# Performance work log

Hardware: AMD Instinct MI355X
Metric: run time of the kernel (lower is better)

The kernel has to match this reference:

```python
import jax, jax.numpy as jnp
import numpy as np

N_NODES = 50000


def _gcn_layer(x, src, dst, W, b, n_nodes):
    # x: [N, Cin] -> linear -> [N, Cout]
    h = x @ W.T + b
    # degree over destination (col) index, including self loops
    deg = jax.ops.segment_sum(jnp.ones(src.shape[0], dtype=x.dtype), dst,
                              num_segments=n_nodes)
    dinv = jnp.where(deg > 0, deg ** -0.5, jnp.zeros((), x.dtype))
    norm = dinv[src] * dinv[dst]                      # [E]
    msg = h[src] * norm[:, None]                      # gather + scale
    return jax.ops.segment_sum(msg, dst, num_segments=n_nodes)  # scatter-add


def setup_inputs() -> dict:
    key = jax.random.key(0)
    k1, k2, k3, k4, k5, k6 = jax.random.split(key, 6)
    num_features = 128
    hidden_dim = 128
    n_edges = 1_600_000
    x = jax.random.normal(k1, (N_NODES, num_features), dtype=jnp.float32)
    edge_index = jax.random.randint(k2, (2, n_edges), 0, N_NODES, dtype=jnp.int64)
    bound1 = 1.0 / np.sqrt(num_features)
    W1 = jax.random.uniform(k3, (hidden_dim, num_features), jnp.float32, -bound1, bound1)
    b1 = jax.random.uniform(k4, (hidden_dim,), jnp.float32, -bound1, bound1)
    bound2 = 1.0 / np.sqrt(hidden_dim)
    W2 = jax.random.uniform(k5, (hidden_dim, hidden_dim), jnp.float32, -bound2, bound2)
    b2 = jax.random.uniform(k6, (hidden_dim,), jnp.float32, -bound2, bound2)
    return {"x": x, "edge_index": edge_index, "W1": W1, "b1": b1, "W2": W2, "b2": b2}


def reference(x, edge_index, W1, b1, W2, b2):
    n_nodes = x.shape[0]
    # add_self_loops: append (i, i) for every node
    loops = jnp.arange(n_nodes, dtype=edge_index.dtype)
    src = jnp.concatenate([edge_index[0], loops])
    dst = jnp.concatenate([edge_index[1], loops])
    h = _gcn_layer(x, src, dst, W1, b1, n_nodes)
    h = jax.nn.relu(h)
    # dropout is identity in eval mode (deterministic reference)
    out = _gcn_layer(h, src, dst, W2, b2, n_nodes)
    return out
```

## Files before the change

kernel.cpp:

```cpp
#include <hip/hip_runtime.h>


static constexpr int F = 128;
static constexpr int NR = 128;
static constexpr int CH = 4096;
static constexpr int CAP = 4608;
static constexpr int RMAX = 512;

typedef __attribute__((ext_vector_type(8))) short bf16x8;
typedef __attribute__((ext_vector_type(4))) float f32x4;
typedef __attribute__((ext_vector_type(4))) unsigned short u16x4;

__device__ __forceinline__ unsigned f2b(float x) {
  unsigned u = __float_as_uint(x);
  return (u + 0x7fffu + ((u >> 16) & 1u)) >> 16;
}
__device__ __forceinline__ float b_lo(unsigned u) {
  return __uint_as_float(u << 16);
}
__device__ __forceinline__ float b_hi(unsigned u) {
  return __uint_as_float(u & 0xffff0000u);
}

__global__ void k_initcur(int* __restrict__ gcur, int R) {
  int i = blockIdx.x * blockDim.x + threadIdx.x;
  if (i < R) gcur[i] = i * CAP;
}

__global__ __launch_bounds__(256) void k_part(const int* __restrict__ src,
                                              const int* __restrict__ dst,
                                              int E, int R,
                                              int* __restrict__ gcur,
                                              unsigned* __restrict__ rsorted) {
  __shared__ int h[RMAX];
  __shared__ int cur[RMAX];
  for (int i = threadIdx.x; i < R; i += 256) h[i] = 0;
  __syncthreads();
  const int e0 = blockIdx.x * CH;
  const int e1 = min(e0 + CH, E);
  for (int i = e0 + threadIdx.x; i < e1; i += 256)
    atomicAdd(&h[dst[i] >> 7], 1);
  __syncthreads();
  for (int i = threadIdx.x; i < R; i += 256)
    cur[i] = h[i] ? atomicAdd(&gcur[i], h[i]) : 0;
  __syncthreads();
  for (int i = e0 + threadIdx.x; i < e1; i += 256) {
    const int d = dst[i];
    const int s = src[i];
    const int pos = atomicAdd(&cur[d >> 7], 1);
    rsorted[pos] = ((unsigned)(d & (NR - 1)) << 16) | (unsigned)s;
  }
}

__global__ __launch_bounds__(256) void k_fillR(
    const unsigned* __restrict__ rsorted, const int* __restrict__ gcur,
    int N, int* __restrict__ rowptr, int* __restrict__ rowend,
    float* __restrict__ dinv, unsigned short* __restrict__ csr) {
  __shared__ unsigned seg[CAP];
  __shared__ unsigned seg2[CAP];
  __shared__ int cnt2[256];
  __shared__ int cur2[256];
  __shared__ int cnt[NR];
  __shared__ int sc[NR];
  __shared__ int cur[NR];
  const int r = blockIdx.x;
  const int tid = threadIdx.x;
  const int b = r * CAP;
  int e = gcur[r];
  if (e > b + CAP) e = b + CAP;
  const int len = e - b;

  cnt2[tid] = 0;
  if (tid < NR) cnt[tid] = 0;
  __syncthreads();
  for (int i = tid; i < len; i += 256) {
    const unsigned v = rsorted[b + i];
    seg[i] = v;
    atomicAdd(&cnt2[(v & 0xffffu) >> 8], 1);
    atomicAdd(&cnt[v >> 16], 1);
  }
  __syncthreads();
  const int v2 = cnt2[tid];
  __syncthreads();
#pragma unroll
  for (int off = 1; off < 256; off <<= 1) {
    const int a = (tid >= off) ? cnt2[tid - off] : 0;
    __syncthreads();
    cnt2[tid] += a;
    __syncthreads();
  }
  cur2[tid] = cnt2[tid] - v2;
  if (tid < NR) sc[tid] = cnt[tid];
  __syncthreads();
#pragma unroll
  for (int off = 1; off < NR; off <<= 1) {
    const int a = (tid < NR && tid >= off) ? sc[tid - off] : 0;
    __syncthreads();
    if (tid < NR) sc[tid] += a;
    __syncthreads();
  }
  if (tid < NR) {
    const int excl = sc[tid] - cnt[tid];
    cur[tid] = excl;
    const int node = r * NR + tid;
    if (node < N) {
      rowptr[node] = b + excl;
      rowend[node] = b + excl + cnt[tid];
      dinv[node] = rsqrtf((float)(cnt[tid] + 1));
    }
  }
  __syncthreads();
  for (int i = tid; i < len; i += 256) {
    const unsigned v = seg[i];
    const int p = atomicAdd(&cur2[(v & 0xffffu) >> 8], 1);
    seg2[p] = v;
  }
  __syncthreads();
  for (int i = tid; i < len; i += 256) {
    const unsigned v = seg2[i];
    const int p = atomicAdd(&cur[v >> 16], 1);
    csr[b + p] = (unsigned short)(v & 0xFFFFu);
  }
}

__global__ __launch_bounds__(256) void k_splitW(const float* __restrict__ W,
                                                unsigned short* __restrict__ hi,
                                                unsigned short* __restrict__ lo) {
  const int i = blockIdx.x * 256 + threadIdx.x;
  const int j = i & 7;
  const int lane = (i >> 3) & 63;
  const int f = (i >> 9) & 7;
  const int t = i >> 12;
  const int col = f * 16 + (lane & 15);
  const int k = t * 32 + ((j & 4) << 2) + 4 * (lane >> 4) + (j & 3);
  const float x = W[col * F + k];
  const unsigned h = f2b(x);
  hi[i] = (unsigned short)h;
  lo[i] = (unsigned short)f2b(x - __uint_as_float(h << 16));
}

template <bool PRESPLIT>
__global__ __launch_bounds__(256) void k_gemm_mfma(
    const float* __restrict__ Af32, const unsigned short* __restrict__ Ahi,
    const unsigned short* __restrict__ Alo,
    const unsigned short* __restrict__ Whi, const unsigned short* __restrict__ Wlo,
    const float* __restrict__ bias, const float* __restrict__ dinv,
    unsigned short* __restrict__ hout, int n) {
  const int wid = threadIdx.x >> 6;
  const int lane = threadIdx.x & 63;
  const int r = lane & 15;
  const int g = lane >> 4;
  const int m0 = blockIdx.x * 64 + wid * 16;
  const int arow = m0 + r;

  f32x4 acc[8];
#pragma unroll
  for (int f = 0; f < 8; ++f) acc[f] = (f32x4){0.f, 0.f, 0.f, 0.f};

#pragma unroll
  for (int t = 0; t < 4; ++t) {
    bf16x8 bhi[8], blo[8];
#pragma unroll
    for (int f = 0; f < 8; ++f) {
      const size_t base = (((size_t)t * 8 + f) * 64 + lane) * 8;
      bhi[f] = *(const bf16x8*)(Whi + base);
      blo[f] = *(const bf16x8*)(Wlo + base);
    }
    const int kt = t * 32;
    bf16x8 ahi = (bf16x8){0, 0, 0, 0, 0, 0, 0, 0};
    bf16x8 alo = (bf16x8){0, 0, 0, 0, 0, 0, 0, 0};
    if (arow < n) {
      if (PRESPLIT) {
        const size_t ab = (size_t)arow * F + kt + 4 * g;
        const u16x4 h0 = *(const u16x4*)(Ahi + ab);
        const u16x4 h1 = *(const u16x4*)(Ahi + ab + 16);
        const u16x4 l0 = *(const u16x4*)(Alo + ab);
        const u16x4 l1 = *(const u16x4*)(Alo + ab + 16);
        ahi[0] = (short)h0[0]; ahi[1] = (short)h0[1]; ahi[2] = (short)h0[2]; ahi[3] = (short)h0[3];
        ahi[4] = (short)h1[0]; ahi[5] = (short)h1[1]; ahi[6] = (short)h1[2]; ahi[7] = (short)h1[3];
        alo[0] = (short)l0[0]; alo[1] = (short)l0[1]; alo[2] = (short)l0[2]; alo[3] = (short)l0[3];
        alo[4] = (short)l1[0]; alo[5] = (short)l1[1]; alo[6] = (short)l1[2]; alo[7] = (short)l1[3];
      } else {
        const float4 a0 = *(const float4*)(Af32 + (size_t)arow * F + kt + 4 * g);
        const float4 a1 = *(const float4*)(Af32 + (size_t)arow * F + kt + 16 + 4 * g);
        unsigned h;
        h = f2b(a0.x); ahi[0] = (short)h; alo[0] = (short)f2b(a0.x - __uint_as_float(h << 16));
        h = f2b(a0.y); ahi[1] = (short)h; alo[1] = (short)f2b(a0.y - __uint_as_float(h << 16));
        h = f2b(a0.z); ahi[2] = (short)h; alo[2] = (short)f2b(a0.z - __uint_as_float(h << 16));
        h = f2b(a0.w); ahi[3] = (short)h; alo[3] = (short)f2b(a0.w - __uint_as_float(h << 16));
        h = f2b(a1.x); ahi[4] = (short)h; alo[4] = (short)f2b(a1.x - __uint_as_float(h << 16));
        h = f2b(a1.y); ahi[5] = (short)h; alo[5] = (short)f2b(a1.y - __uint_as_float(h << 16));
        h = f2b(a1.z); ahi[6] = (short)h; alo[6] = (short)f2b(a1.z - __uint_as_float(h << 16));
        h = f2b(a1.w); ahi[7] = (short)h; alo[7] = (short)f2b(a1.w - __uint_as_float(h << 16));
      }
    }
#pragma unroll
    for (int f = 0; f < 8; ++f) {
      acc[f] = __builtin_amdgcn_mfma_f32_16x16x32_bf16(ahi, bhi[f], acc[f], 0, 0, 0);
      acc[f] = __builtin_amdgcn_mfma_f32_16x16x32_bf16(ahi, blo[f], acc[f], 0, 0, 0);
      acc[f] = __builtin_amdgcn_mfma_f32_16x16x32_bf16(alo, bhi[f], acc[f], 0, 0, 0);
    }
  }

  int orow[4];
  float dv[4];
#pragma unroll
  for (int j = 0; j < 4; ++j) {
    orow[j] = m0 + 4 * g + j;
    dv[j] = (orow[j] < n) ? dinv[orow[j]] : 0.f;
  }
#pragma unroll
  for (int f = 0; f < 8; ++f) {
    const int col = f * 16 + r;
    const float bv = bias[col];
#pragma unroll
    for (int j = 0; j < 4; ++j) {
      if (orow[j] < n)
        hout[(size_t)orow[j] * F + col] = (unsigned short)f2b((acc[f][j] + bv) * dv[j]);
    }
  }
}

template <int MODE>
__global__ __launch_bounds__(256) void k_pull(
    const int* __restrict__ rowptr, const int* __restrict__ rowend,
    const unsigned short* __restrict__ csr, const uint2* __restrict__ h,
    const float* __restrict__ dinv, unsigned short* __restrict__ ahi,
    unsigned short* __restrict__ alo, float* __restrict__ fout, int n) {
  const int wid = (blockIdx.x * blockDim.x + threadIdx.x) >> 6;
  if (wid >= n) return;
  const int lane = threadIdx.x & 63;
  const int half = lane >> 5;
  const int l32 = lane & 31;
  const int beg = rowptr[wid];
  const int end = rowend[wid];

  float4 acc = make_float4(0.f, 0.f, 0.f, 0.f);
  if (half == 0) {
    const uint2 u = h[(size_t)wid * 32 + l32];
    acc.x = b_lo(u.x); acc.y = b_hi(u.x);
    acc.z = b_lo(u.y); acc.w = b_hi(u.y);
  }

  int k = beg + half;
  for (; k + 6 < end; k += 8) {
    const int s0 = csr[k];
    const int s1 = csr[k + 2];
    const int s2 = csr[k + 4];
    const int s3 = csr[k + 6];
    const uint2 u0 = h[(size_t)s0 * 32 + l32];
    const uint2 u1 = h[(size_t)s1 * 32 + l32];
    const uint2 u2 = h[(size_t)s2 * 32 + l32];
    const uint2 u3 = h[(size_t)s3 * 32 + l32];
    acc.x += b_lo(u0.x) + b_lo(u1.x) + b_lo(u2.x) + b_lo(u3.x);
    acc.y += b_hi(u0.x) + b_hi(u1.x) + b_hi(u2.x) + b_hi(u3.x);
    acc.z += b_lo(u0.y) + b_lo(u1.y) + b_lo(u2.y) + b_lo(u3.y);
    acc.w += b_hi(u0.y) + b_hi(u1.y) + b_hi(u2.y) + b_hi(u3.y);
  }
  for (; k < end; k += 2) {
    const uint2 u = h[(size_t)csr[k] * 32 + l32];
    acc.x += b_lo(u.x);
    acc.y += b_hi(u.x);
    acc.z += b_lo(u.y);
    acc.w += b_hi(u.y);
  }

  acc.x += __shfl_xor(acc.x, 32, 64);
  acc.y += __shfl_xor(acc.y, 32, 64);
  acc.z += __shfl_xor(acc.z, 32, 64);
  acc.w += __shfl_xor(acc.w, 32, 64);

  if (half == 0) {
    const float dv = dinv[wid];
    float rx = acc.x * dv;
    float ry = acc.y * dv;
    float rz = acc.z * dv;
    float rw = acc.w * dv;
    if (MODE == 0) {
      rx = fmaxf(rx, 0.f);
      ry = fmaxf(ry, 0.f);
      rz = fmaxf(rz, 0.f);
      rw = fmaxf(rw, 0.f);
      u16x4 hv, lv;
      unsigned u;
      u = f2b(rx); hv[0] = (unsigned short)u; lv[0] = (unsigned short)f2b(rx - __uint_as_float(u << 16));
      u = f2b(ry); hv[1] = (unsigned short)u; lv[1] = (unsigned short)f2b(ry - __uint_as_float(u << 16));
      u = f2b(rz); hv[2] = (unsigned short)u; lv[2] = (unsigned short)f2b(rz - __uint_as_float(u << 16));
      u = f2b(rw); hv[3] = (unsigned short)u; lv[3] = (unsigned short)f2b(rw - __uint_as_float(u << 16));
      *(u16x4*)(ahi + (size_t)wid * F + l32 * 4) = hv;
      *(u16x4*)(alo + (size_t)wid * F + l32 * 4) = lv;
    } else {
      float4 rv;
      rv.x = rx; rv.y = ry; rv.z = rz; rv.w = rw;
      *(float4*)(fout + (size_t)wid * F + l32 * 4) = rv;
    }
  }
}

extern "C" void kernel_launch(void* const* d_in, const int* in_sizes, int n_in,
                              void* d_out, int out_size, void* d_ws, size_t ws_size,
                              hipStream_t stream) {
  const float* x  = (const float*)d_in[0];
  const int*   ei = (const int*)d_in[1];
  const float* W1 = (const float*)d_in[2];
  const float* b1 = (const float*)d_in[3];
  const float* W2 = (const float*)d_in[4];
  const float* b2 = (const float*)d_in[5];

  const int N = in_sizes[0] / F;
  const int E = in_sizes[1] / 2;
  const int* src = ei;
  const int* dst = ei + E;
  const int R = (N + NR - 1) / NR;
  const int C = (E + CH - 1) / CH;

  char* ws = (char*)d_ws;
  int*            gcur    = (int*)(ws + (8u << 10));
  float*          dinv    = (float*)(ws + (16u << 10));
  int*            rowptr  = (int*)(ws + (256u << 10));
  int*            rowend  = (int*)(ws + (512u << 10));
  unsigned short* Whi1    = (unsigned short*)(ws + (768u << 10));
  unsigned short* Wlo1    = (unsigned short*)(ws + (800u << 10));
  unsigned short* Whi2    = (unsigned short*)(ws + (832u << 10));
  unsigned short* Wlo2    = (unsigned short*)(ws + (864u << 10));
  unsigned*       rsorted = (unsigned*)(ws + (1u << 20));
  unsigned short* csr     = (unsigned short*)(ws + (9u << 20));
  unsigned short* hbuf    = (unsigned short*)(ws + (16u << 20));
  unsigned short* Ahi     = (unsigned short*)(ws + (32u << 20));
  unsigned short* Alo     = (unsigned short*)(ws + (45u << 20));
  float*          out     = (float*)d_out;

  const int B = 256;
  const int gemmBlocks = (N + 63) / 64;
  const int pullBlocks = (N * 64 + B - 1) / B;

  k_initcur<<<(R + 255) / 256, B, 0, stream>>>(gcur, R);
  k_part<<<C, B, 0, stream>>>(src, dst, E, R, gcur, rsorted);
  k_fillR<<<R, B, 0, stream>>>(rsorted, gcur, N, rowptr, rowend, dinv, csr);
  k_splitW<<<64, B, 0, stream>>>(W1, Whi1, Wlo1);
  k_splitW<<<64, B, 0, stream>>>(W2, Whi2, Wlo2);

  k_gemm_mfma<false><<<gemmBlocks, B, 0, stream>>>(x, nullptr, nullptr, Whi1,
                                                   Wlo1, b1, dinv, hbuf, N);
  k_pull<0><<<pullBlocks, B, 0, stream>>>(rowptr, rowend, csr,
                                          (const uint2*)hbuf, dinv, Ahi, Alo,
                                          nullptr, N);

  k_gemm_mfma<true><<<gemmBlocks, B, 0, stream>>>(nullptr, Ahi, Alo, Whi2,
                                                  Wlo2, b2, dinv, hbuf, N);
  k_pull<1><<<pullBlocks, B, 0, stream>>>(rowptr, rowend, csr,
                                          (const uint2*)hbuf, dinv, nullptr,
                                          nullptr, out, N);
}
```

Before: 205.2 us.

## Split pull feature dimension across block pairs and drop secondary CSR sort

The pull kernel now gives each wave one node and half of the 128 features, using 16 lanes per edge slot and four edge slots per wave. Blocks are interleaved so that both feature halves of the same node group run close together. This raises edge-level parallelism per node and keeps gathers within 128-byte rows. The fillR kernel drops the second counting sort by source bucket, which removes shared-memory passes but loses the source-ordered CSR layout that may have helped gather locality.

```diff
diff --git a/kernel.cpp b/kernel.cpp
--- a/kernel.cpp
+++ b/kernel.cpp
@@ -57,9 +57,6 @@
     int N, int* __restrict__ rowptr, int* __restrict__ rowend,
     float* __restrict__ dinv, unsigned short* __restrict__ csr) {
   __shared__ unsigned seg[CAP];
-  __shared__ unsigned seg2[CAP];
-  __shared__ int cnt2[256];
-  __shared__ int cur2[256];
   __shared__ int cnt[NR];
   __shared__ int sc[NR];
   __shared__ int cur[NR];
@@ -70,26 +67,14 @@
   if (e > b + CAP) e = b + CAP;
   const int len = e - b;
 
-  cnt2[tid] = 0;
   if (tid < NR) cnt[tid] = 0;
   __syncthreads();
   for (int i = tid; i < len; i += 256) {
     const unsigned v = rsorted[b + i];
     seg[i] = v;
-    atomicAdd(&cnt2[(v & 0xffffu) >> 8], 1);
     atomicAdd(&cnt[v >> 16], 1);
   }
   __syncthreads();
-  const int v2 = cnt2[tid];
-  __syncthreads();
-#pragma unroll
-  for (int off = 1; off < 256; off <<= 1) {
-    const int a = (tid >= off) ? cnt2[tid - off] : 0;
-    __syncthreads();
-    cnt2[tid] += a;
-    __syncthreads();
-  }
-  cur2[tid] = cnt2[tid] - v2;
   if (tid < NR) sc[tid] = cnt[tid];
   __syncthreads();
 #pragma unroll
@@ -112,12 +97,6 @@
   __syncthreads();
   for (int i = tid; i < len; i += 256) {
     const unsigned v = seg[i];
-    const int p = atomicAdd(&cur2[(v & 0xffffu) >> 8], 1);
-    seg2[p] = v;
-  }
-  __syncthreads();
-  for (int i = tid; i < len; i += 256) {
-    const unsigned v = seg2[i];
     const int p = atomicAdd(&cur[v >> 16], 1);
     csr[b + p] = (unsigned short)(v & 0xFFFFu);
   }
@@ -227,51 +206,60 @@
     const unsigned short* __restrict__ csr, const uint2* __restrict__ h,
     const float* __restrict__ dinv, unsigned short* __restrict__ ahi,
     unsigned short* __restrict__ alo, float* __restrict__ fout, int n) {
-  const int wid = (blockIdx.x * blockDim.x + threadIdx.x) >> 6;
-  if (wid >= n) return;
+  const int b = blockIdx.x;
+  const int hf = (b & 7) >> 2;
+  const int g = ((b >> 3) << 2) | (b & 3);
+  const int node = g * 4 + (threadIdx.x >> 6);
+  if (node >= n) return;
   const int lane = threadIdx.x & 63;
-  const int half = lane >> 5;
-  const int l32 = lane & 31;
-  const int beg = rowptr[wid];
-  const int end = rowend[wid];
+  const int slot = lane >> 4;
+  const int li = lane & 15;
+  const uint2* __restrict__ hq = h + hf * 16;
+
+  const int beg = rowptr[node];
+  const int end = rowend[node];
 
   float4 acc = make_float4(0.f, 0.f, 0.f, 0.f);
-  if (half == 0) {
-    const uint2 u = h[(size_t)wid * 32 + l32];
+  if (slot == 0) {
+    const uint2 u = hq[(size_t)node * 32 + li];
     acc.x = b_lo(u.x); acc.y = b_hi(u.x);
     acc.z = b_lo(u.y); acc.w = b_hi(u.y);
   }
 
-  int k = beg + half;
-  for (; k + 6 < end; k += 8) {
+  int k = beg + slot;
+  for (; k + 12 < end; k += 16) {
     const int s0 = csr[k];
-    const int s1 = csr[k + 2];
-    const int s2 = csr[k + 4];
-    const int s3 = csr[k + 6];
-    const uint2 u0 = h[(size_t)s0 * 32 + l32];
-    const uint2 u1 = h[(size_t)s1 * 32 + l32];
-    const uint2 u2 = h[(size_t)s2 * 32 + l32];
-    const uint2 u3 = h[(size_t)s3 * 32 + l32];
+    const int s1 = csr[k + 4];
+    const int s2 = csr[k + 8];
+    const int s3 = csr[k + 12];
+    const uint2 u0 = hq[(size_t)s0 * 32 + li];
+    const uint2 u1 = hq[(size_t)s1 * 32 + li];
+    const uint2 u2 = hq[(size_t)s2 * 32 + li];
+    const uint2 u3 = hq[(size_t)s3 * 32 + li];
     acc.x += b_lo(u0.x) + b_lo(u1.x) + b_lo(u2.x) + b_lo(u3.x);
     acc.y += b_hi(u0.x) + b_hi(u1.x) + b_hi(u2.x) + b_hi(u3.x);
     acc.z += b_lo(u0.y) + b_lo(u1.y) + b_lo(u2.y) + b_lo(u3.y);
     acc.w += b_hi(u0.y) + b_hi(u1.y) + b_hi(u2.y) + b_hi(u3.y);
   }
-  for (; k < end; k += 2) {
-    const uint2 u = h[(size_t)csr[k] * 32 + l32];
+  for (; k < end; k += 4) {
+    const uint2 u = hq[(size_t)csr[k] * 32 + li];
     acc.x += b_lo(u.x);
     acc.y += b_hi(u.x);
     acc.z += b_lo(u.y);
     acc.w += b_hi(u.y);
   }
 
+  acc.x += __shfl_xor(acc.x, 16, 64);
+  acc.y += __shfl_xor(acc.y, 16, 64);
+  acc.z += __shfl_xor(acc.z, 16, 64);
+  acc.w += __shfl_xor(acc.w, 16, 64);
   acc.x += __shfl_xor(acc.x, 32, 64);
   acc.y += __shfl_xor(acc.y, 32, 64);
   acc.z += __shfl_xor(acc.z, 32, 64);
   acc.w += __shfl_xor(acc.w, 32, 64);
 
-  if (half == 0) {
-    const float dv = dinv[wid];
+  if (slot == 0) {
+    const float dv = dinv[node];
     float rx = acc.x * dv;
     float ry = acc.y * dv;
     float rz = acc.z * dv;
@@ -287,12 +275,13 @@
       u = f2b(ry); hv[1] = (unsigned short)u; lv[1] = (unsigned short)f2b(ry - __uint_as_float(u << 16));
       u = f2b(rz); hv[2] = (unsigned short)u; lv[2] = (unsigned short)f2b(rz - __uint_as_float(u << 16));
       u = f2b(rw); hv[3] = (unsigned short)u; lv[3] = (unsigned short)f2b(rw - __uint_as_float(u << 16));
-      *(u16x4*)(ahi + (size_t)wid * F + l32 * 4) = hv;
-      *(u16x4*)(alo + (size_t)wid * F + l32 * 4) = lv;
+      const size_t o = (size_t)node * F + hf * 64 + li * 4;
+      *(u16x4*)(ahi + o) = hv;
+      *(u16x4*)(alo + o) = lv;
     } else {
       float4 rv;
       rv.x = rx; rv.y = ry; rv.z = rz; rv.w = rw;
-      *(float4*)(fout + (size_t)wid * F + l32 * 4) = rv;
+      *(float4*)(fout + (size_t)node * F + hf * 64 + li * 4) = rv;
     }
   }
 }
@@ -332,7 +321,8 @@
 
   const int B = 256;
   const int gemmBlocks = (N + 63) / 64;
-  const int pullBlocks = (N * 64 + B - 1) / B;
+  const int groups = (N + 3) / 4;
+  const int pullBlocks = 8 * ((groups + 3) / 4);
 
   k_initcur<<<(R + 255) / 256, B, 0, stream>>>(gcur, R);
   k_part<<<C, B, 0, stream>>>(src, dst, E, R, gcur, rsorted);
```

Result: slower. 219.0 us (+6.8%).

## Drop secondary radix pass in fillR and split GEMM columns across waves

Applied to the files above, without the earlier changes.

The CSR fill kernel no longer performs a pre-sort by source-node high byte, so the second shared-memory buffer, its histogram and its scan are gone, and the per-row placement is done straight from the loaded segment. This removes a scan and a full LDS scatter pass, but within each row the source order becomes arbitrary instead of roughly sorted, which may hurt gather locality in the pull kernels. The GEMM now gives each block 16 rows, with each of the four waves computing two of the eight 16-column tiles instead of all eight for its own 16 rows. That cuts registers per wave and raises the block count, at the cost of loading the A tile four times per block.

```diff
diff --git a/kernel.cpp b/kernel.cpp
--- a/kernel.cpp
+++ b/kernel.cpp
@@ -57,9 +57,6 @@
     int N, int* __restrict__ rowptr, int* __restrict__ rowend,
     float* __restrict__ dinv, unsigned short* __restrict__ csr) {
   __shared__ unsigned seg[CAP];
-  __shared__ unsigned seg2[CAP];
-  __shared__ int cnt2[256];
-  __shared__ int cur2[256];
   __shared__ int cnt[NR];
   __shared__ int sc[NR];
   __shared__ int cur[NR];
@@ -70,26 +67,14 @@
   if (e > b + CAP) e = b + CAP;
   const int len = e - b;
 
-  cnt2[tid] = 0;
   if (tid < NR) cnt[tid] = 0;
   __syncthreads();
   for (int i = tid; i < len; i += 256) {
     const unsigned v = rsorted[b + i];
     seg[i] = v;
-    atomicAdd(&cnt2[(v & 0xffffu) >> 8], 1);
     atomicAdd(&cnt[v >> 16], 1);
   }
   __syncthreads();
-  const int v2 = cnt2[tid];
-  __syncthreads();
-#pragma unroll
-  for (int off = 1; off < 256; off <<= 1) {
-    const int a = (tid >= off) ? cnt2[tid - off] : 0;
-    __syncthreads();
-    cnt2[tid] += a;
-    __syncthreads();
-  }
-  cur2[tid] = cnt2[tid] - v2;
   if (tid < NR) sc[tid] = cnt[tid];
   __syncthreads();
 #pragma unroll
@@ -112,12 +97,6 @@
   __syncthreads();
   for (int i = tid; i < len; i += 256) {
     const unsigned v = seg[i];
-    const int p = atomicAdd(&cur2[(v & 0xffffu) >> 8], 1);
-    seg2[p] = v;
-  }
-  __syncthreads();
-  for (int i = tid; i < len; i += 256) {
-    const unsigned v = seg2[i];
     const int p = atomicAdd(&cur[v >> 16], 1);
     csr[b + p] = (unsigned short)(v & 0xFFFFu);
   }
@@ -150,22 +129,21 @@
   const int lane = threadIdx.x & 63;
   const int r = lane & 15;
   const int g = lane >> 4;
-  const int m0 = blockIdx.x * 64 + wid * 16;
+  const int m0 = blockIdx.x * 16;
   const int arow = m0 + r;
-
-  f32x4 acc[8];
-#pragma unroll
-  for (int f = 0; f < 8; ++f) acc[f] = (f32x4){0.f, 0.f, 0.f, 0.f};
+  const int f0 = 2 * wid;
+
+  f32x4 acc0 = (f32x4){0.f, 0.f, 0.f, 0.f};
+  f32x4 acc1 = (f32x4){0.f, 0.f, 0.f, 0.f};
 
 #pragma unroll
   for (int t = 0; t < 4; ++t) {
-    bf16x8 bhi[8], blo[8];
-#pragma unroll
-    for (int f = 0; f < 8; ++f) {
-      const size_t base = (((size_t)t * 8 + f) * 64 + lane) * 8;
-      bhi[f] = *(const bf16x8*)(Whi + base);
-      blo[f] = *(const bf16x8*)(Wlo + base);
-    }
+    const size_t base0 = (((size_t)t * 8 + f0) * 64 + lane) * 8;
+    const size_t base1 = (((size_t)t * 8 + f0 + 1) * 64 + lane) * 8;
+    const bf16x8 bhi0 = *(const bf16x8*)(Whi + base0);
+    const bf16x8 blo0 = *(const bf16x8*)(Wlo + base0);
+    const bf16x8 bhi1 = *(const bf16x8*)(Whi + base1);
+    const bf16x8 blo1 = *(const bf16x8*)(Wlo + base1);
     const int kt = t * 32;
     bf16x8 ahi = (bf16x8){0, 0, 0, 0, 0, 0, 0, 0};
     bf16x8 alo = (bf16x8){0, 0, 0, 0, 0, 0, 0, 0};
@@ -194,12 +172,12 @@
         h = f2b(a1.w); ahi[7] = (short)h; alo[7] = (short)f2b(a1.w - __uint_as_float(h << 16));
       }
     }
-#pragma unroll
-    for (int f = 0; f < 8; ++f) {
-      acc[f] = __builtin_amdgcn_mfma_f32_16x16x32_bf16(ahi, bhi[f], acc[f], 0, 0, 0);
-      acc[f] = __builtin_amdgcn_mfma_f32_16x16x32_bf16(ahi, blo[f], acc[f], 0, 0, 0);
-      acc[f] = __builtin_amdgcn_mfma_f32_16x16x32_bf16(alo, bhi[f], acc[f], 0, 0, 0);
-    }
+    acc0 = __builtin_amdgcn_mfma_f32_16x16x32_bf16(ahi, bhi0, acc0, 0, 0, 0);
+    acc0 = __builtin_amdgcn_mfma_f32_16x16x32_bf16(ahi, blo0, acc0, 0, 0, 0);
+    acc0 = __builtin_amdgcn_mfma_f32_16x16x32_bf16(alo, bhi0, acc0, 0, 0, 0);
+    acc1 = __builtin_amdgcn_mfma_f32_16x16x32_bf16(ahi, bhi1, acc1, 0, 0, 0);
+    acc1 = __builtin_amdgcn_mfma_f32_16x16x32_bf16(ahi, blo1, acc1, 0, 0, 0);
+    acc1 = __builtin_amdgcn_mfma_f32_16x16x32_bf16(alo, bhi1, acc1, 0, 0, 0);
   }
 
   int orow[4];
@@ -209,14 +187,15 @@
     orow[j] = m0 + 4 * g + j;
     dv[j] = (orow[j] < n) ? dinv[orow[j]] : 0.f;
   }
+  const int col0 = f0 * 16 + r;
+  const int col1 = col0 + 16;
+  const float bv0 = bias[col0];
+  const float bv1 = bias[col1];
 #pragma unroll
-  for (int f = 0; f < 8; ++f) {
-    const int col = f * 16 + r;
-    const float bv = bias[col];
-#pragma unroll
-    for (int j = 0; j < 4; ++j) {
-      if (orow[j] < n)
-        hout[(size_t)orow[j] * F + col] = (unsigned short)f2b((acc[f][j] + bv) * dv[j]);
+  for (int j = 0; j < 4; ++j) {
+    if (orow[j] < n) {
+      hout[(size_t)orow[j] * F + col0] = (unsigned short)f2b((acc0[j] + bv0) * dv[j]);
+      hout[(size_t)orow[j] * F + col1] = (unsigned short)f2b((acc1[j] + bv1) * dv[j]);
     }
   }
 }
@@ -331,7 +310,7 @@
   float*          out     = (float*)d_out;
 
   const int B = 256;
-  const int gemmBlocks = (N + 63) / 64;
+  const int gemmBlocks = (N + 15) / 16;
   const int pullBlocks = (N * 64 + B - 1) / B;
 
   k_initcur<<<(R + 255) / 256, B, 0, stream>>>(gcur, R);
```

Result: slower. 211.6 us (+3.1%).

## Stage weight tiles in LDS for GEMM and drop secondary source sort in CSR fill

Applied to the files above, without the earlier changes.

The GEMM kernel now loads each k-slice of the split bf16 weights into shared memory once per block, and each wave reads its fragments from LDS. Previously every wave loaded them from global memory into registers. The change aims to cut redundant global and L2 traffic and register pressure, at the cost of two barriers per k-step and a loss of unrolling. Separately, the CSR fill kernel no longer pre-sorts each segment by source high byte before bucketing by row. That removes a scan, a scatter pass and shared memory, but edges within a row may lose their source-ordered locality for later gathers.

```diff
diff --git a/kernel.cpp b/kernel.cpp
--- a/kernel.cpp
+++ b/kernel.cpp
@@ -57,9 +57,6 @@
     int N, int* __restrict__ rowptr, int* __restrict__ rowend,
     float* __restrict__ dinv, unsigned short* __restrict__ csr) {
   __shared__ unsigned seg[CAP];
-  __shared__ unsigned seg2[CAP];
-  __shared__ int cnt2[256];
-  __shared__ int cur2[256];
   __shared__ int cnt[NR];
   __shared__ int sc[NR];
   __shared__ int cur[NR];
@@ -70,26 +67,14 @@
   if (e > b + CAP) e = b + CAP;
   const int len = e - b;
 
-  cnt2[tid] = 0;
   if (tid < NR) cnt[tid] = 0;
   __syncthreads();
   for (int i = tid; i < len; i += 256) {
     const unsigned v = rsorted[b + i];
     seg[i] = v;
-    atomicAdd(&cnt2[(v & 0xffffu) >> 8], 1);
     atomicAdd(&cnt[v >> 16], 1);
   }
   __syncthreads();
-  const int v2 = cnt2[tid];
-  __syncthreads();
-#pragma unroll
-  for (int off = 1; off < 256; off <<= 1) {
-    const int a = (tid >= off) ? cnt2[tid - off] : 0;
-    __syncthreads();
-    cnt2[tid] += a;
-    __syncthreads();
-  }
-  cur2[tid] = cnt2[tid] - v2;
   if (tid < NR) sc[tid] = cnt[tid];
   __syncthreads();
 #pragma unroll
@@ -112,12 +97,6 @@
   __syncthreads();
   for (int i = tid; i < len; i += 256) {
     const unsigned v = seg[i];
-    const int p = atomicAdd(&cur2[(v & 0xffffu) >> 8], 1);
-    seg2[p] = v;
-  }
-  __syncthreads();
-  for (int i = tid; i < len; i += 256) {
-    const unsigned v = seg2[i];
     const int p = atomicAdd(&cur[v >> 16], 1);
     csr[b + p] = (unsigned short)(v & 0xFFFFu);
   }
@@ -146,8 +125,11 @@
     const unsigned short* __restrict__ Whi, const unsigned short* __restrict__ Wlo,
     const float* __restrict__ bias, const float* __restrict__ dinv,
     unsigned short* __restrict__ hout, int n) {
-  const int wid = threadIdx.x >> 6;
-  const int lane = threadIdx.x & 63;
+  __shared__ unsigned short sWhi[4096];
+  __shared__ unsigned short sWlo[4096];
+  const int tid = threadIdx.x;
+  const int wid = tid >> 6;
+  const int lane = tid & 63;
   const int r = lane & 15;
   const int g = lane >> 4;
   const int m0 = blockIdx.x * 64 + wid * 16;
@@ -157,15 +139,20 @@
 #pragma unroll
   for (int f = 0; f < 8; ++f) acc[f] = (f32x4){0.f, 0.f, 0.f, 0.f};
 
-#pragma unroll
   for (int t = 0; t < 4; ++t) {
-    bf16x8 bhi[8], blo[8];
-#pragma unroll
-    for (int f = 0; f < 8; ++f) {
-      const size_t base = (((size_t)t * 8 + f) * 64 + lane) * 8;
-      bhi[f] = *(const bf16x8*)(Whi + base);
-      blo[f] = *(const bf16x8*)(Wlo + base);
-    }
+    __syncthreads();
+    {
+      const uint4* __restrict__ gh = (const uint4*)(Whi + t * 4096);
+      const uint4* __restrict__ gl = (const uint4*)(Wlo + t * 4096);
+      uint4* dh = (uint4*)sWhi;
+      uint4* dl = (uint4*)sWlo;
+      dh[tid] = gh[tid];
+      dh[tid + 256] = gh[tid + 256];
+      dl[tid] = gl[tid];
+      dl[tid + 256] = gl[tid + 256];
+    }
+    __syncthreads();
+
     const int kt = t * 32;
     bf16x8 ahi = (bf16x8){0, 0, 0, 0, 0, 0, 0, 0};
     bf16x8 alo = (bf16x8){0, 0, 0, 0, 0, 0, 0, 0};
@@ -196,9 +183,11 @@
     }
 #pragma unroll
     for (int f = 0; f < 8; ++f) {
-      acc[f] = __builtin_amdgcn_mfma_f32_16x16x32_bf16(ahi, bhi[f], acc[f], 0, 0, 0);
-      acc[f] = __builtin_amdgcn_mfma_f32_16x16x32_bf16(ahi, blo[f], acc[f], 0, 0, 0);
-      acc[f] = __builtin_amdgcn_mfma_f32_16x16x32_bf16(alo, bhi[f], acc[f], 0, 0, 0);
+      const bf16x8 bhi = *(const bf16x8*)(sWhi + (f * 64 + lane) * 8);
+      const bf16x8 blo = *(const bf16x8*)(sWlo + (f * 64 + lane) * 8);
+      acc[f] = __builtin_amdgcn_mfma_f32_16x16x32_bf16(ahi, bhi, acc[f], 0, 0, 0);
+      acc[f] = __builtin_amdgcn_mfma_f32_16x16x32_bf16(ahi, blo, acc[f], 0, 0, 0);
+      acc[f] = __builtin_amdgcn_mfma_f32_16x16x32_bf16(alo, bhi, acc[f], 0, 0, 0);
     }
   }
 
```

After: 192.0 us. 1.07x faster.
